# Kernel tuning notes

Measured on AMD Instinct MI355X. Metric: run time of the kernel, lower is better.

The kernel has to match this reference:

```python
import jax, jax.numpy as jnp
import numpy as np

D = 4096          # in = out features of the quantized linear
K = 128           # n_quantize (codebook size)
B, S = 4, 4096    # batch, seq_len


def setup_inputs() -> dict:
    key = jax.random.key(0)
    k1, k2, k3, k4 = jax.random.split(key, 4)
    x = jax.random.normal(k1, (B, S, D), dtype=jnp.float32)
    quantized_vectors = jax.random.normal(k2, (D, K), dtype=jnp.float32)
    assignments = jax.random.randint(k3, (D,), 0, K, dtype=jnp.int32)
    bias = jax.random.normal(k4, (D,), dtype=jnp.float32)
    return {"x": x, "quantized_vectors": quantized_vectors,
            "assignments": assignments, "bias": bias}


def reference(x, quantized_vectors, assignments, bias):
    orig_shape = x.shape
    x_flat = x.reshape(-1, quantized_vectors.shape[0])          # [T, D]
    # row-gather the codebook then skinny matmul: [T, D] @ [D, K] -> [T, K]
    gathered = jnp.take(quantized_vectors, assignments, axis=0)  # [D, K]
    qm = jnp.einsum('ij,jk->ik', x_flat, gathered)               # [T, K]
    # column gather back to D outputs, add bias
    out = jnp.take(qm, assignments, axis=1) + bias[None, :]      # [T, D]
    return out.reshape(orig_shape)
```

## Files before the change

### kernel.cpp

```cpp
#include <hip/hip_runtime.h>

#define DD 4096
#define KK 128
#define MAXHC 48
#define XROW 4100
#define QVC_OFF 24832

__global__ void vq_build(const float* __restrict__ qv,
                         const int* __restrict__ assign,
                         unsigned short* __restrict__ perm2,
                         int* __restrict__ maxh,
                         float4* __restrict__ qvC) {
    const int tid = threadIdx.x;

    if (blockIdx.x == 1) {
        for (int idx = tid; idx < 4096; idx += 256) {
            const int c4 = idx >> 7;
            const int k  = idx & (KK - 1);
            float4 v;
            v.x = qv[(4 * c4 + 0) * KK + k];
            v.y = qv[(4 * c4 + 1) * KK + k];
            v.z = qv[(4 * c4 + 2) * KK + k];
            v.w = qv[(4 * c4 + 3) * KK + k];
            qvC[idx] = v;
        }
        return;
    }

    __shared__ int cnt[KK];
    __shared__ int off[KK];

    if (tid < KK) cnt[tid] = 0;
    for (int i = tid; i < MAXHC * 256; i += 256)
        perm2[i] = (unsigned short)DD;
    __syncthreads();

    for (int j = tid; j < DD; j += 256)
        atomicAdd(&cnt[assign[j]], 1);
    __syncthreads();

    if (tid == 0) {
        int m = 0;
        for (int c = 0; c < KK; ++c) {
            off[c] = 0;
            int h = (cnt[c] + 1) >> 1;
            if (h > m) m = h;
        }
        *maxh = (m < MAXHC) ? m : MAXHC;
    }
    __syncthreads();

    for (int j = tid; j < DD; j += 256) {
        const int c = assign[j];
        const int p = atomicAdd(&off[c], 1);
        const int i = p >> 1;
        const int th = 2 * c + (p & 1);
        if (i < MAXHC)
            perm2[(i >> 1) * 512 + th * 2 + (i & 1)] = (unsigned short)j;
    }
}

__global__ __launch_bounds__(256) void vq_main(
    const float* __restrict__ x,
    const int*   __restrict__ assign,
    const float* __restrict__ bias,
    const unsigned int* __restrict__ pu,
    const int* __restrict__ maxh,
    const float4* __restrict__ qvC,
    float* __restrict__ out)
{
    __shared__ float xl[2 * XROW];
    __shared__ float xs[2 * KK];
    __shared__ float qm2[2 * KK];

    const int t0  = blockIdx.x * 2;
    const int tid = threadIdx.x;

    const float4* r0 = reinterpret_cast<const float4*>(x + (size_t)t0 * DD);
    const float4* r1 = reinterpret_cast<const float4*>(x + (size_t)(t0 + 1) * DD);
    float4* xl40 = reinterpret_cast<float4*>(xl);
    float4* xl41 = reinterpret_cast<float4*>(xl + XROW);
    #pragma unroll
    for (int i = 0; i < 4; ++i) {
        xl40[tid + i * 256] = r0[tid + i * 256];
        xl41[tid + i * 256] = r1[tid + i * 256];
    }
    if (tid == 0) { xl[DD] = 0.0f; xl[XROW + DD] = 0.0f; }
    __syncthreads();

    {
        const int mh2 = (*maxh + 1) >> 1;
        float a0 = 0.0f, a1 = 0.0f;
        for (int ii = 0; ii < mh2; ++ii) {
            const unsigned int pp = pu[ii * 256 + tid];
            const int i0 = pp & 0xFFFFu;
            const int i1 = pp >> 16;
            a0 += xl[i0];
            a0 += xl[i1];
            a1 += xl[XROW + i0];
            a1 += xl[XROW + i1];
        }
        a0 += __shfl_xor(a0, 1);
        a1 += __shfl_xor(a1, 1);
        if ((tid & 1) == 0) {
            xs[tid >> 1]      = a0;
            xs[KK + (tid >> 1)] = a1;
        }
    }
    __syncthreads();

    {
        const int k  = tid & (KK - 1);
        const int tt = tid >> 7;
        const float4* xs4 = reinterpret_cast<const float4*>(xs + tt * KK);
        float ax = 0.f, ay = 0.f, az = 0.f, aw = 0.f;
        #pragma unroll 8
        for (int c4 = 0; c4 < 32; ++c4) {
            const float4 q = qvC[c4 * KK + k];
            const float4 v = xs4[c4];
            ax += q.x * v.x;
            ay += q.y * v.y;
            az += q.z * v.z;
            aw += q.w * v.w;
        }
        qm2[2 * k + tt] = (ax + ay) + (az + aw);
    }
    __syncthreads();

    const int4*   a4   = reinterpret_cast<const int4*>(assign);
    const float4* b4   = reinterpret_cast<const float4*>(bias);
    const float2* qmf2 = reinterpret_cast<const float2*>(qm2);
    float4* o0 = reinterpret_cast<float4*>(out + (size_t)t0 * DD);
    float4* o1 = reinterpret_cast<float4*>(out + (size_t)(t0 + 1) * DD);
    #pragma unroll
    for (int i = 0; i < 4; ++i) {
        const int idx = tid + i * 256;
        const int4   a = a4[idx];
        const float4 b = b4[idx];
        const float2 qx = qmf2[a.x];
        const float2 qy = qmf2[a.y];
        const float2 qz = qmf2[a.z];
        const float2 qw = qmf2[a.w];
        float4 s0, s1;
        s0.x = qx.x + b.x;  s1.x = qx.y + b.x;
        s0.y = qy.x + b.y;  s1.y = qy.y + b.y;
        s0.z = qz.x + b.z;  s1.z = qz.y + b.z;
        s0.w = qw.x + b.w;  s1.w = qw.y + b.w;
        o0[idx] = s0;
        o1[idx] = s1;
    }
}

extern "C" void kernel_launch(void* const* d_in, const int* in_sizes, int n_in,
                              void* d_out, int out_size, void* d_ws, size_t ws_size,
                              hipStream_t stream) {
    const float* x      = (const float*)d_in[0];
    const float* qv     = (const float*)d_in[1];
    const int*   assign = (const int*)d_in[2];
    const float* bias   = (const float*)d_in[3];
    float*       out    = (float*)d_out;

    unsigned short* perm2 = (unsigned short*)d_ws;
    int*    maxh = (int*)((char*)d_ws + MAXHC * 256 * sizeof(unsigned short));
    float4* qvC  = (float4*)((char*)d_ws + QVC_OFF);

    const int T = in_sizes[0] / DD;

    vq_build<<<dim3(2), dim3(256), 0, stream>>>(qv, assign, perm2, maxh, qvC);
    vq_main<<<dim3(T / 2), dim3(256), 0, stream>>>(
        x, assign, bias, (const unsigned int*)perm2, maxh, qvC, out);
}
```

Measured before the change: 458.5 us.

## Process four tokens per block with fp16-packed x rows in LDS

Each block now handles four tokens instead of two. The x rows are converted to half precision and packed in pairs into 32-bit LDS words, so LDS use stays about the same and each gather load fetches two tokens. The codebook matmul is reorganised so every qvC load is reused across four tokens, split over thread pairs and combined with a shuffle. The aim is to halve the codebook and assign/bias traffic per token and to cut LDS gather instructions. The cost is fp16 rounding of x before the cluster sums, which changes numerical accuracy.

```diff
diff --git a/kernel.cpp b/kernel.cpp
--- a/kernel.cpp
+++ b/kernel.cpp
@@ -1,10 +1,17 @@
 #include <hip/hip_runtime.h>
+#include <hip/hip_fp16.h>
 
 #define DD 4096
 #define KK 128
 #define MAXHC 48
-#define XROW 4100
+#define XL2 4112
 #define QVC_OFF 24832
+
+union H2 { unsigned int u; __half2 h; };
+
+static __device__ __forceinline__ unsigned int pkh2(float lo, float hi) {
+    H2 r; r.h = __floats2half2_rn(lo, hi); return r.u;
+}
 
 __global__ void vq_build(const float* __restrict__ qv,
                          const int* __restrict__ assign,
@@ -69,85 +76,125 @@
     const float4* __restrict__ qvC,
     float* __restrict__ out)
 {
-    __shared__ float xl[2 * XROW];
-    __shared__ float xs[2 * KK];
-    __shared__ float qm2[2 * KK];
-
-    const int t0  = blockIdx.x * 2;
+    __shared__ unsigned int xp[2 * XL2];
+    __shared__ float xs[4 * KK];
+    __shared__ float4 qm4[KK];
+
+    const int t0  = blockIdx.x * 4;
     const int tid = threadIdx.x;
 
-    const float4* r0 = reinterpret_cast<const float4*>(x + (size_t)t0 * DD);
-    const float4* r1 = reinterpret_cast<const float4*>(x + (size_t)(t0 + 1) * DD);
-    float4* xl40 = reinterpret_cast<float4*>(xl);
-    float4* xl41 = reinterpret_cast<float4*>(xl + XROW);
-    #pragma unroll
-    for (int i = 0; i < 4; ++i) {
-        xl40[tid + i * 256] = r0[tid + i * 256];
-        xl41[tid + i * 256] = r1[tid + i * 256];
-    }
-    if (tid == 0) { xl[DD] = 0.0f; xl[XROW + DD] = 0.0f; }
+    {
+        const float4* r0 = reinterpret_cast<const float4*>(x + (size_t)(t0 + 0) * DD);
+        const float4* r1 = reinterpret_cast<const float4*>(x + (size_t)(t0 + 1) * DD);
+        const float4* r2 = reinterpret_cast<const float4*>(x + (size_t)(t0 + 2) * DD);
+        const float4* r3 = reinterpret_cast<const float4*>(x + (size_t)(t0 + 3) * DD);
+        uint4* pa = reinterpret_cast<uint4*>(xp);
+        uint4* pb = reinterpret_cast<uint4*>(xp + XL2);
+        #pragma unroll
+        for (int i = 0; i < 4; ++i) {
+            const int idx = tid + i * 256;
+            const float4 a = r0[idx];
+            const float4 b = r1[idx];
+            const float4 c = r2[idx];
+            const float4 d = r3[idx];
+            uint4 wa, wb;
+            wa.x = pkh2(a.x, b.x); wa.y = pkh2(a.y, b.y);
+            wa.z = pkh2(a.z, b.z); wa.w = pkh2(a.w, b.w);
+            wb.x = pkh2(c.x, d.x); wb.y = pkh2(c.y, d.y);
+            wb.z = pkh2(c.z, d.z); wb.w = pkh2(c.w, d.w);
+            pa[idx] = wa;
+            pb[idx] = wb;
+        }
+        if (tid == 0) { xp[DD] = 0u; xp[XL2 + DD] = 0u; }
+    }
     __syncthreads();
 
     {
         const int mh2 = (*maxh + 1) >> 1;
-        float a0 = 0.0f, a1 = 0.0f;
+        float s0 = 0.f, s1 = 0.f, s2 = 0.f, s3 = 0.f;
         for (int ii = 0; ii < mh2; ++ii) {
             const unsigned int pp = pu[ii * 256 + tid];
             const int i0 = pp & 0xFFFFu;
             const int i1 = pp >> 16;
-            a0 += xl[i0];
-            a0 += xl[i1];
-            a1 += xl[XROW + i0];
-            a1 += xl[XROW + i1];
-        }
-        a0 += __shfl_xor(a0, 1);
-        a1 += __shfl_xor(a1, 1);
+            H2 wa0, wb0, wa1, wb1;
+            wa0.u = xp[i0];        wb0.u = xp[XL2 + i0];
+            wa1.u = xp[i1];        wb1.u = xp[XL2 + i1];
+            s0 += __low2float(wa0.h);  s1 += __high2float(wa0.h);
+            s2 += __low2float(wb0.h);  s3 += __high2float(wb0.h);
+            s0 += __low2float(wa1.h);  s1 += __high2float(wa1.h);
+            s2 += __low2float(wb1.h);  s3 += __high2float(wb1.h);
+        }
+        s0 += __shfl_xor(s0, 1);
+        s1 += __shfl_xor(s1, 1);
+        s2 += __shfl_xor(s2, 1);
+        s3 += __shfl_xor(s3, 1);
         if ((tid & 1) == 0) {
-            xs[tid >> 1]      = a0;
-            xs[KK + (tid >> 1)] = a1;
-        }
-    }
-    __syncthreads();
-
-    {
-        const int k  = tid & (KK - 1);
-        const int tt = tid >> 7;
-        const float4* xs4 = reinterpret_cast<const float4*>(xs + tt * KK);
-        float ax = 0.f, ay = 0.f, az = 0.f, aw = 0.f;
-        #pragma unroll 8
-        for (int c4 = 0; c4 < 32; ++c4) {
-            const float4 q = qvC[c4 * KK + k];
-            const float4 v = xs4[c4];
-            ax += q.x * v.x;
-            ay += q.y * v.y;
-            az += q.z * v.z;
-            aw += q.w * v.w;
-        }
-        qm2[2 * k + tt] = (ax + ay) + (az + aw);
-    }
-    __syncthreads();
-
-    const int4*   a4   = reinterpret_cast<const int4*>(assign);
-    const float4* b4   = reinterpret_cast<const float4*>(bias);
-    const float2* qmf2 = reinterpret_cast<const float2*>(qm2);
-    float4* o0 = reinterpret_cast<float4*>(out + (size_t)t0 * DD);
-    float4* o1 = reinterpret_cast<float4*>(out + (size_t)(t0 + 1) * DD);
-    #pragma unroll
-    for (int i = 0; i < 4; ++i) {
-        const int idx = tid + i * 256;
-        const int4   a = a4[idx];
-        const float4 b = b4[idx];
-        const float2 qx = qmf2[a.x];
-        const float2 qy = qmf2[a.y];
-        const float2 qz = qmf2[a.z];
-        const float2 qw = qmf2[a.w];
-        float4 s0, s1;
-        s0.x = qx.x + b.x;  s1.x = qx.y + b.x;
-        s0.y = qy.x + b.y;  s1.y = qy.y + b.y;
-        s0.z = qz.x + b.z;  s1.z = qz.y + b.z;
-        s0.w = qw.x + b.w;  s1.w = qw.y + b.w;
-        o0[idx] = s0;
-        o1[idx] = s1;
+            const int c = tid >> 1;
+            xs[c]          = s0;
+            xs[KK + c]     = s1;
+            xs[2 * KK + c] = s2;
+            xs[3 * KK + c] = s3;
+        }
+    }
+    __syncthreads();
+
+    {
+        const int k = tid >> 1;
+        const int h = tid & 1;
+        const float4* xsf4 = reinterpret_cast<const float4*>(xs);
+        float4 acc[4];
+        acc[0] = acc[1] = acc[2] = acc[3] = make_float4(0.f, 0.f, 0.f, 0.f);
+        #pragma unroll 4
+        for (int c4 = 0; c4 < 16; ++c4) {
+            const int cg = h * 16 + c4;
+            const float4 q = qvC[cg * KK + k];
+            #pragma unroll
+            for (int tt = 0; tt < 4; ++tt) {
+                const float4 v = xsf4[tt * 32 + cg];
+                acc[tt].x += q.x * v.x;
+                acc[tt].y += q.y * v.y;
+                acc[tt].z += q.z * v.z;
+                acc[tt].w += q.w * v.w;
+            }
+        }
+        float r0 = (acc[0].x + acc[0].y) + (acc[0].z + acc[0].w);
+        float r1 = (acc[1].x + acc[1].y) + (acc[1].z + acc[1].w);
+        float r2 = (acc[2].x + acc[2].y) + (acc[2].z + acc[2].w);
+        float r3 = (acc[3].x + acc[3].y) + (acc[3].z + acc[3].w);
+        r0 += __shfl_xor(r0, 1);
+        r1 += __shfl_xor(r1, 1);
+        r2 += __shfl_xor(r2, 1);
+        r3 += __shfl_xor(r3, 1);
+        if (h == 0) qm4[k] = make_float4(r0, r1, r2, r3);
+    }
+    __syncthreads();
+
+    {
+        const int4*   a4 = reinterpret_cast<const int4*>(assign);
+        const float4* b4 = reinterpret_cast<const float4*>(bias);
+        float4* o0 = reinterpret_cast<float4*>(out + (size_t)(t0 + 0) * DD);
+        float4* o1 = reinterpret_cast<float4*>(out + (size_t)(t0 + 1) * DD);
+        float4* o2 = reinterpret_cast<float4*>(out + (size_t)(t0 + 2) * DD);
+        float4* o3 = reinterpret_cast<float4*>(out + (size_t)(t0 + 3) * DD);
+        #pragma unroll
+        for (int i = 0; i < 4; ++i) {
+            const int idx = tid + i * 256;
+            const int4   a = a4[idx];
+            const float4 b = b4[idx];
+            const float4 qx = qm4[a.x];
+            const float4 qy = qm4[a.y];
+            const float4 qz = qm4[a.z];
+            const float4 qw = qm4[a.w];
+            float4 s;
+            s.x = qx.x + b.x; s.y = qy.x + b.y; s.z = qz.x + b.z; s.w = qw.x + b.w;
+            o0[idx] = s;
+            s.x = qx.y + b.x; s.y = qy.y + b.y; s.z = qz.y + b.z; s.w = qw.y + b.w;
+            o1[idx] = s;
+            s.x = qx.z + b.x; s.y = qy.z + b.y; s.z = qz.z + b.z; s.w = qw.z + b.w;
+            o2[idx] = s;
+            s.x = qx.w + b.x; s.y = qy.w + b.y; s.z = qz.w + b.z; s.w = qw.w + b.w;
+            o3[idx] = s;
+        }
     }
 }
 
@@ -167,6 +214,6 @@
     const int T = in_sizes[0] / DD;
 
     vq_build<<<dim3(2), dim3(256), 0, stream>>>(qv, assign, perm2, maxh, qvC);
-    vq_main<<<dim3(T / 2), dim3(256), 0, stream>>>(
+    vq_main<<<dim3(T / 4), dim3(256), 0, stream>>>(
         x, assign, bias, (const unsigned int*)perm2, maxh, qvC, out);
 }
```

Result: no change. 461.7 us (+0.7%).

## Pack two token rows as fp16 pairs in LDS and split the codebook matvec

Applied to the files above, without the earlier changes.

The staged x rows for the two tokens are now packed as interleaved half2 values, so LDS use drops from about 32KB to about 16KB per block, and launch bounds now request 8 blocks per SM. The gather-sum step then does one LDS load per index for both tokens instead of two. The small matvec is redistributed so each thread pair handles both tokens over half the columns, loading each codebook float4 once for two tokens. The change converts activations to fp16 before summation, which loses precision, and whether that stays within tolerance is uncertain.

```diff
diff --git a/kernel.cpp b/kernel.cpp
--- a/kernel.cpp
+++ b/kernel.cpp
@@ -1,10 +1,17 @@
 #include <hip/hip_runtime.h>
+#include <hip/hip_fp16.h>
 
 #define DD 4096
 #define KK 128
 #define MAXHC 48
-#define XROW 4100
+#define XL2 4112
 #define QVC_OFF 24832
+
+union H2 { unsigned int u; __half2 h; };
+
+static __device__ __forceinline__ unsigned int pkh2(float lo, float hi) {
+    H2 r; r.h = __floats2half2_rn(lo, hi); return r.u;
+}
 
 __global__ void vq_build(const float* __restrict__ qv,
                          const int* __restrict__ assign,
@@ -60,7 +67,7 @@
     }
 }
 
-__global__ __launch_bounds__(256) void vq_main(
+__global__ __launch_bounds__(256, 8) void vq_main(
     const float* __restrict__ x,
     const int*   __restrict__ assign,
     const float* __restrict__ bias,
@@ -69,85 +76,105 @@
     const float4* __restrict__ qvC,
     float* __restrict__ out)
 {
-    __shared__ float xl[2 * XROW];
+    __shared__ unsigned int xp[XL2];
     __shared__ float xs[2 * KK];
     __shared__ float qm2[2 * KK];
 
     const int t0  = blockIdx.x * 2;
     const int tid = threadIdx.x;
 
-    const float4* r0 = reinterpret_cast<const float4*>(x + (size_t)t0 * DD);
-    const float4* r1 = reinterpret_cast<const float4*>(x + (size_t)(t0 + 1) * DD);
-    float4* xl40 = reinterpret_cast<float4*>(xl);
-    float4* xl41 = reinterpret_cast<float4*>(xl + XROW);
-    #pragma unroll
-    for (int i = 0; i < 4; ++i) {
-        xl40[tid + i * 256] = r0[tid + i * 256];
-        xl41[tid + i * 256] = r1[tid + i * 256];
+    {
+        const float4* r0 = reinterpret_cast<const float4*>(x + (size_t)(t0 + 0) * DD);
+        const float4* r1 = reinterpret_cast<const float4*>(x + (size_t)(t0 + 1) * DD);
+        uint4* pa = reinterpret_cast<uint4*>(xp);
+        #pragma unroll
+        for (int i = 0; i < 4; ++i) {
+            const int idx = tid + i * 256;
+            const float4 a = r0[idx];
+            const float4 b = r1[idx];
+            uint4 wa;
+            wa.x = pkh2(a.x, b.x); wa.y = pkh2(a.y, b.y);
+            wa.z = pkh2(a.z, b.z); wa.w = pkh2(a.w, b.w);
+            pa[idx] = wa;
+        }
+        if (tid == 0) xp[DD] = 0u;
     }
-    if (tid == 0) { xl[DD] = 0.0f; xl[XROW + DD] = 0.0f; }
     __syncthreads();
 
     {
         const int mh2 = (*maxh + 1) >> 1;
-        float a0 = 0.0f, a1 = 0.0f;
+        float s0 = 0.f, s1 = 0.f;
         for (int ii = 0; ii < mh2; ++ii) {
             const unsigned int pp = pu[ii * 256 + tid];
             const int i0 = pp & 0xFFFFu;
             const int i1 = pp >> 16;
-            a0 += xl[i0];
-            a0 += xl[i1];
-            a1 += xl[XROW + i0];
-            a1 += xl[XROW + i1];
+            H2 w0, w1;
+            w0.u = xp[i0];
+            w1.u = xp[i1];
+            s0 += __low2float(w0.h);  s1 += __high2float(w0.h);
+            s0 += __low2float(w1.h);  s1 += __high2float(w1.h);
         }
-        a0 += __shfl_xor(a0, 1);
-        a1 += __shfl_xor(a1, 1);
+        s0 += __shfl_xor(s0, 1);
+        s1 += __shfl_xor(s1, 1);
         if ((tid & 1) == 0) {
-            xs[tid >> 1]      = a0;
-            xs[KK + (tid >> 1)] = a1;
+            const int c = tid >> 1;
+            xs[c]      = s0;
+            xs[KK + c] = s1;
         }
     }
     __syncthreads();
 
     {
-        const int k  = tid & (KK - 1);
-        const int tt = tid >> 7;
-        const float4* xs4 = reinterpret_cast<const float4*>(xs + tt * KK);
-        float ax = 0.f, ay = 0.f, az = 0.f, aw = 0.f;
-        #pragma unroll 8
-        for (int c4 = 0; c4 < 32; ++c4) {
-            const float4 q = qvC[c4 * KK + k];
-            const float4 v = xs4[c4];
-            ax += q.x * v.x;
-            ay += q.y * v.y;
-            az += q.z * v.z;
-            aw += q.w * v.w;
+        const int k = tid >> 1;
+        const int h = tid & 1;
+        const float4* xsf4 = reinterpret_cast<const float4*>(xs);
+        float4 a0 = make_float4(0.f, 0.f, 0.f, 0.f);
+        float4 a1 = make_float4(0.f, 0.f, 0.f, 0.f);
+        #pragma unroll 4
+        for (int c4 = 0; c4 < 16; ++c4) {
+            const int cg = h * 16 + c4;
+            const float4 q  = qvC[cg * KK + k];
+            const float4 v0 = xsf4[cg];
+            const float4 v1 = xsf4[32 + cg];
+            a0.x += q.x * v0.x;  a0.y += q.y * v0.y;
+            a0.z += q.z * v0.z;  a0.w += q.w * v0.w;
+            a1.x += q.x * v1.x;  a1.y += q.y * v1.y;
+            a1.z += q.z * v1.z;  a1.w += q.w * v1.w;
         }
-        qm2[2 * k + tt] = (ax + ay) + (az + aw);
+        float r0 = (a0.x + a0.y) + (a0.z + a0.w);
+        float r1 = (a1.x + a1.y) + (a1.z + a1.w);
+        r0 += __shfl_xor(r0, 1);
+        r1 += __shfl_xor(r1, 1);
+        if (h == 0) {
+            qm2[2 * k]     = r0;
+            qm2[2 * k + 1] = r1;
+        }
     }
     __syncthreads();
 
-    const int4*   a4   = reinterpret_cast<const int4*>(assign);
-    const float4* b4   = reinterpret_cast<const float4*>(bias);
-    const float2* qmf2 = reinterpret_cast<const float2*>(qm2);
-    float4* o0 = reinterpret_cast<float4*>(out + (size_t)t0 * DD);
-    float4* o1 = reinterpret_cast<float4*>(out + (size_t)(t0 + 1) * DD);
-    #pragma unroll
-    for (int i = 0; i < 4; ++i) {
-        const int idx = tid + i * 256;
-        const int4   a = a4[idx];
-        const float4 b = b4[idx];
-        const float2 qx = qmf2[a.x];
-        const float2 qy = qmf2[a.y];
-        const float2 qz = qmf2[a.z];
-        const float2 qw = qmf2[a.w];
-        float4 s0, s1;
-        s0.x = qx.x + b.x;  s1.x = qx.y + b.x;
-        s0.y = qy.x + b.y;  s1.y = qy.y + b.y;
-        s0.z = qz.x + b.z;  s1.z = qz.y + b.z;
-        s0.w = qw.x + b.w;  s1.w = qw.y + b.w;
-        o0[idx] = s0;
-        o1[idx] = s1;
+    {
+        const int4*   a4   = reinterpret_cast<const int4*>(assign);
+        const float4* b4   = reinterpret_cast<const float4*>(bias);
+        const float2* qmf2 = reinterpret_cast<const float2*>(qm2);
+        float4* o0 = reinterpret_cast<float4*>(out + (size_t)(t0 + 0) * DD);
+        float4* o1 = reinterpret_cast<float4*>(out + (size_t)(t0 + 1) * DD);
+        #pragma unroll
+        for (int i = 0; i < 4; ++i) {
+            const int idx = tid + i * 256;
+            const int4   a = a4[idx];
+            const float4 b = b4[idx];
+            const float2 qx = qmf2[a.x];
+            const float2 qy = qmf2[a.y];
+            const float2 qz = qmf2[a.z];
+            const float2 qw = qmf2[a.w];
+            float4 s0, s1;
+            s0.x = qx.x + b.x;  s1.x = qx.y + b.x;
+            s0.y = qy.x + b.y;  s1.y = qy.y + b.y;
+            s0.z = qz.x + b.z;  s1.z = qz.y + b.z;
+            s0.w = qw.x + b.w;  s1.w = qw.y + b.w;
+            o0[idx] = s0;
+            o1[idx] = s1;
+        }
     }
 }
 
```

New measurement: 483.7 us. 1.06x slower.
